# Kernel tuning notes

Measured on AMD Instinct MI355X. Metric: run time of the kernel, lower is better.

The kernel has to match this reference:

```python
import jax, jax.numpy as jnp
import numpy as np
from jax import lax

DT = 0.001            # Euler step_size (forward default)
STEPS_PER_OUT = 5     # t spacing 0.005 / dt 0.001 (t grid aligned with step grid)


def setup_inputs() -> dict:
    key = jax.random.key(0)
    ks = jax.random.split(key, 6)
    B, K, C, F, H = 8192, 2, 2, 64, 64
    D = C * F
    x0 = jax.random.normal(ks[0], (B, K, C, F), dtype=jnp.float32)
    t = jnp.arange(51, dtype=jnp.float32) * 0.005  # 51 output times, aligned to dt grid
    # Kaiming-ish small init so tanh stays in a sane range over 250 Euler steps
    W1 = jax.random.normal(ks[1], (D, H), dtype=jnp.float32) / jnp.sqrt(jnp.float32(D))
    b1 = jax.random.normal(ks[2], (H,), dtype=jnp.float32) * 0.01
    W2 = jax.random.normal(ks[3], (H, D), dtype=jnp.float32) / jnp.sqrt(jnp.float32(H))
    b2 = jax.random.normal(ks[4], (D,), dtype=jnp.float32) * 0.01
    return {"x0": x0, "t": t, "W1": W1, "b1": b1, "W2": W2, "b2": b2}


def reference(x0, t, W1, b1, W2, b2):
    B, K, C, F = x0.shape
    T = t.shape[0]

    def dydt(y):  # tiny 2-layer tanh MLP derivative, y: [B, C*F]
        return jnp.tanh(y @ W1 + b1) @ W2 + b2

    def euler_substep(i, y):
        return y + DT * dydt(y)

    def interval(y, _):
        # STEPS_PER_OUT fixed Euler steps between consecutive output times
        y = lax.fori_loop(0, STEPS_PER_OUT, euler_substep, y)
        return y, y

    y0 = x0.reshape(B, K, C * F)[:, 0]            # flatten(start_dim=-2) then [:, 0]
    _, ys = lax.scan(interval, y0, None, length=T - 1)  # [T-1, B, D]
    out = jnp.concatenate([y0[None], ys], axis=0)       # [T, B, D]
    out = jnp.transpose(out, (1, 0, 2))                 # permute(1,0,2) -> [B, T, D]
    return out.reshape(B, T, C, F)                      # unflatten -> [B, T, C, F]
```

## Files before the change

### kernel.cpp

```cpp
#include <hip/hip_runtime.h>
#include <hip/hip_bf16.h>


typedef __attribute__((ext_vector_type(8))) short bf16x8;
typedef __attribute__((ext_vector_type(4))) float floatx4;

static __device__ __forceinline__ short f2bf(float f) {
    return __builtin_bit_cast(short, (__bf16)f);
}

static __device__ __forceinline__ unsigned pack2(float a, float b) {
    unsigned short lo = __builtin_bit_cast(unsigned short, (__bf16)a);
    unsigned short hi = __builtin_bit_cast(unsigned short, (__bf16)b);
    return (unsigned)lo | ((unsigned)hi << 16);
}

static __device__ __forceinline__ float tanh_fast(float x) {
    float e = __expf(2.0f * x);
    return 1.0f - 2.0f * __builtin_amdgcn_rcpf(1.0f + e);
}

#define YP 136
#define HP 72

__global__ __launch_bounds__(256, 1) void node_kernel(
    const float* __restrict__ x0, const float* __restrict__ W1,
    const float* __restrict__ b1, const float* __restrict__ W2,
    const float* __restrict__ b2, float* __restrict__ out)
{
    __shared__ __align__(16) unsigned short Yld[16 * YP];
    __shared__ __align__(16) unsigned short Hld[16 * HP];

    const int tid  = threadIdx.x;
    const int w    = tid >> 6;
    const int lane = tid & 63;
    const int n    = lane & 15;
    const int q    = lane >> 4;
    const int row  = (blockIdx.x << 4) + n;

    bf16x8 w1f[4];
    #pragma unroll
    for (int kt = 0; kt < 4; ++kt) {
        const int m  = w * 16 + n;
        const int k0 = kt * 32 + q * 8;
        bf16x8 v;
        #pragma unroll
        for (int j = 0; j < 8; ++j) v[j] = f2bf(W1[(k0 + j) * 64 + m]);
        w1f[kt] = v;
    }
    bf16x8 w2f[2][2];
    #pragma unroll
    for (int i = 0; i < 2; ++i) {
        #pragma unroll
        for (int kt = 0; kt < 2; ++kt) {
            const int m  = w * 32 + i * 16 + n;
            const int k0 = kt * 32 + q * 8;
            bf16x8 v;
            #pragma unroll
            for (int j = 0; j < 8; ++j) v[j] = f2bf(W2[(k0 + j) * 128 + m]);
            w2f[i][kt] = v;
        }
    }

    floatx4 b1f, b2f[2];
    #pragma unroll
    for (int r = 0; r < 4; ++r) b1f[r] = b1[w * 16 + q * 4 + r];
    #pragma unroll
    for (int i = 0; i < 2; ++i)
        #pragma unroll
        for (int r = 0; r < 4; ++r) b2f[i][r] = b2[w * 32 + i * 16 + q * 4 + r];

    floatx4 y[2];
    #pragma unroll
    for (int i = 0; i < 2; ++i)
        #pragma unroll
        for (int r = 0; r < 4; ++r)
            y[i][r] = x0[row * 256 + w * 32 + i * 16 + q * 4 + r];

    #pragma unroll
    for (int i = 0; i < 2; ++i) {
        uint2 p;
        p.x = pack2(y[i][0], y[i][1]);
        p.y = pack2(y[i][2], y[i][3]);
        *reinterpret_cast<uint2*>(&Yld[n * YP + w * 32 + i * 16 + q * 4]) = p;
        *reinterpret_cast<floatx4*>(out + row * 51 * 128 + w * 32 + i * 16 + q * 4) = y[i];
    }
    __syncthreads();

    for (int ti = 1; ti <= 50; ++ti) {
        #pragma unroll
        for (int ss = 0; ss < 5; ++ss) {
            bf16x8 yb[4];
            #pragma unroll
            for (int kt = 0; kt < 4; ++kt)
                yb[kt] = __builtin_bit_cast(bf16x8,
                    *reinterpret_cast<const uint4*>(&Yld[n * YP + kt * 32 + q * 8]));
            floatx4 accA = b1f;
            floatx4 accB = {0.0f, 0.0f, 0.0f, 0.0f};
            accA = __builtin_amdgcn_mfma_f32_16x16x32_bf16(w1f[0], yb[0], accA, 0, 0, 0);
            accB = __builtin_amdgcn_mfma_f32_16x16x32_bf16(w1f[1], yb[1], accB, 0, 0, 0);
            accA = __builtin_amdgcn_mfma_f32_16x16x32_bf16(w1f[2], yb[2], accA, 0, 0, 0);
            accB = __builtin_amdgcn_mfma_f32_16x16x32_bf16(w1f[3], yb[3], accB, 0, 0, 0);

            {
                float t0 = tanh_fast(accA[0] + accB[0]);
                float t1 = tanh_fast(accA[1] + accB[1]);
                float t2 = tanh_fast(accA[2] + accB[2]);
                float t3 = tanh_fast(accA[3] + accB[3]);
                uint2 p;
                p.x = pack2(t0, t1);
                p.y = pack2(t2, t3);
                *reinterpret_cast<uint2*>(&Hld[n * HP + w * 16 + q * 4]) = p;
            }
            __syncthreads();

            bf16x8 hb[2];
            #pragma unroll
            for (int kt = 0; kt < 2; ++kt)
                hb[kt] = __builtin_bit_cast(bf16x8,
                    *reinterpret_cast<const uint4*>(&Hld[n * HP + kt * 32 + q * 8]));
            floatx4 acc2[2] = { b2f[0], b2f[1] };
            #pragma unroll
            for (int kt = 0; kt < 2; ++kt)
                #pragma unroll
                for (int i = 0; i < 2; ++i)
                    acc2[i] = __builtin_amdgcn_mfma_f32_16x16x32_bf16(
                        w2f[i][kt], hb[kt], acc2[i], 0, 0, 0);

            #pragma unroll
            for (int i = 0; i < 2; ++i) {
                #pragma unroll
                for (int r = 0; r < 4; ++r)
                    y[i][r] = fmaf(0.001f, acc2[i][r], y[i][r]);
                uint2 p;
                p.x = pack2(y[i][0], y[i][1]);
                p.y = pack2(y[i][2], y[i][3]);
                *reinterpret_cast<uint2*>(&Yld[n * YP + w * 32 + i * 16 + q * 4]) = p;
            }
            __syncthreads();
        }
        #pragma unroll
        for (int i = 0; i < 2; ++i)
            *reinterpret_cast<floatx4*>(
                out + row * 51 * 128 + ti * 128 + w * 32 + i * 16 + q * 4) = y[i];
    }
}

extern "C" void kernel_launch(void* const* d_in, const int* in_sizes, int n_in,
                              void* d_out, int out_size, void* d_ws, size_t ws_size,
                              hipStream_t stream) {
    const float* x0 = (const float*)d_in[0];
    const float* W1 = (const float*)d_in[2];
    const float* b1 = (const float*)d_in[3];
    const float* W2 = (const float*)d_in[4];
    const float* b2 = (const float*)d_in[5];
    float* out = (float*)d_out;

    node_kernel<<<dim3(512), dim3(256), 0, stream>>>(x0, W1, b1, W2, b2, out);
}
```

Baseline: 307.5 us.

## Integrate Euler recurrence in hidden space using precomputed W2·W1 product

Rewrites the Euler update in the 64-wide pre-activation space: z_{k+1} = z_k + dt*(tanh(z_k)·W2W1 + b2W1), using a product matrix computed by a new small precompute kernel. The full 128-wide output y is reconstructed only once per output interval from the summed tanh activations, which halves the inner-step MFMA count and drops the per-step Y write. It also adds XOR-swizzled LDS layouts and double-buffered activation storage, which removes one barrier per substep. The trade-offs are an extra kernel launch and different rounding, since the product is rounded to bf16 and the summed activations are stored in bf16.

```diff
diff --git a/kernel.cpp b/kernel.cpp
--- a/kernel.cpp
+++ b/kernel.cpp
@@ -4,6 +4,8 @@
 
 typedef __attribute__((ext_vector_type(8))) short bf16x8;
 typedef __attribute__((ext_vector_type(4))) float floatx4;
+
+__device__ float g_w21[64 * 64 + 64];
 
 static __device__ __forceinline__ short f2bf(float f) {
     return __builtin_bit_cast(short, (__bf16)f);
@@ -20,16 +22,42 @@
     return 1.0f - 2.0f * __builtin_amdgcn_rcpf(1.0f + e);
 }
 
-#define YP 136
-#define HP 72
+__global__ __launch_bounds__(64) void precompute_kernel(
+    const float* __restrict__ W1, const float* __restrict__ W2,
+    const float* __restrict__ b2)
+{
+    const int hout = threadIdx.x;
+    const int hin  = blockIdx.x;
+    float a0 = 0.f, a1 = 0.f, a2 = 0.f, a3 = 0.f;
+    if (hin < 64) {
+        #pragma unroll 4
+        for (int d = 0; d < 128; d += 4) {
+            a0 = fmaf(W2[hin * 128 + d + 0], W1[(d + 0) * 64 + hout], a0);
+            a1 = fmaf(W2[hin * 128 + d + 1], W1[(d + 1) * 64 + hout], a1);
+            a2 = fmaf(W2[hin * 128 + d + 2], W1[(d + 2) * 64 + hout], a2);
+            a3 = fmaf(W2[hin * 128 + d + 3], W1[(d + 3) * 64 + hout], a3);
+        }
+        g_w21[hin * 64 + hout] = (a0 + a1) + (a2 + a3);
+    } else {
+        #pragma unroll 4
+        for (int d = 0; d < 128; d += 4) {
+            a0 = fmaf(b2[d + 0], W1[(d + 0) * 64 + hout], a0);
+            a1 = fmaf(b2[d + 1], W1[(d + 1) * 64 + hout], a1);
+            a2 = fmaf(b2[d + 2], W1[(d + 2) * 64 + hout], a2);
+            a3 = fmaf(b2[d + 3], W1[(d + 3) * 64 + hout], a3);
+        }
+        g_w21[4096 + hout] = (a0 + a1) + (a2 + a3);
+    }
+}
 
 __global__ __launch_bounds__(256, 1) void node_kernel(
     const float* __restrict__ x0, const float* __restrict__ W1,
     const float* __restrict__ b1, const float* __restrict__ W2,
     const float* __restrict__ b2, float* __restrict__ out)
 {
-    __shared__ __align__(16) unsigned short Yld[16 * YP];
-    __shared__ __align__(16) unsigned short Hld[16 * HP];
+    __shared__ __align__(16) unsigned short Ald[2][16 * 64];
+    __shared__ __align__(16) unsigned short Sld[16 * 64];
+    __shared__ __align__(16) unsigned short Yld[16 * 128];
 
     const int tid  = threadIdx.x;
     const int w    = tid >> 6;
@@ -37,16 +65,17 @@
     const int n    = lane & 15;
     const int q    = lane >> 4;
     const int row  = (blockIdx.x << 4) + n;
-
-    bf16x8 w1f[4];
-    #pragma unroll
-    for (int kt = 0; kt < 4; ++kt) {
+    const int swz  = n & 7;
+
+    bf16x8 w21f[2];
+    #pragma unroll
+    for (int kt = 0; kt < 2; ++kt) {
         const int m  = w * 16 + n;
         const int k0 = kt * 32 + q * 8;
         bf16x8 v;
         #pragma unroll
-        for (int j = 0; j < 8; ++j) v[j] = f2bf(W1[(k0 + j) * 64 + m]);
-        w1f[kt] = v;
+        for (int j = 0; j < 8; ++j) v[j] = f2bf(g_w21[(k0 + j) * 64 + m]);
+        w21f[kt] = v;
     }
     bf16x8 w2f[2][2];
     #pragma unroll
@@ -62,13 +91,17 @@
         }
     }
 
-    floatx4 b1f, b2f[2];
-    #pragma unroll
-    for (int r = 0; r < 4; ++r) b1f[r] = b1[w * 16 + q * 4 + r];
+    floatx4 cf, b1f, b2f5[2];
+    #pragma unroll
+    for (int r = 0; r < 4; ++r) {
+        cf[r]  = g_w21[4096 + w * 16 + q * 4 + r];
+        b1f[r] = b1[w * 16 + q * 4 + r];
+    }
     #pragma unroll
     for (int i = 0; i < 2; ++i)
         #pragma unroll
-        for (int r = 0; r < 4; ++r) b2f[i][r] = b2[w * 32 + i * 16 + q * 4 + r];
+        for (int r = 0; r < 4; ++r)
+            b2f5[i][r] = 5.0f * b2[w * 32 + i * 16 + q * 4 + r];
 
     floatx4 y[2];
     #pragma unroll
@@ -79,70 +112,90 @@
 
     #pragma unroll
     for (int i = 0; i < 2; ++i) {
+        const int j0 = 4 * w + 2 * i + (q >> 1);
         uint2 p;
         p.x = pack2(y[i][0], y[i][1]);
         p.y = pack2(y[i][2], y[i][3]);
-        *reinterpret_cast<uint2*>(&Yld[n * YP + w * 32 + i * 16 + q * 4]) = p;
+        *reinterpret_cast<uint2*>(&Yld[n * 128 + (j0 ^ swz) * 8 + (q & 1) * 4]) = p;
         *reinterpret_cast<floatx4*>(out + row * 51 * 128 + w * 32 + i * 16 + q * 4) = y[i];
     }
     __syncthreads();
 
+    floatx4 z = b1f;
+    #pragma unroll
+    for (int kt = 0; kt < 4; ++kt) {
+        bf16x8 yb = __builtin_bit_cast(bf16x8, *reinterpret_cast<const uint4*>(
+            &Yld[n * 128 + ((kt * 4 + q) ^ swz) * 8]));
+        const int m  = w * 16 + n;
+        const int k0 = kt * 32 + q * 8;
+        bf16x8 w1t;
+        #pragma unroll
+        for (int j = 0; j < 8; ++j) w1t[j] = f2bf(W1[(k0 + j) * 64 + m]);
+        z = __builtin_amdgcn_mfma_f32_16x16x32_bf16(w1t, yb, z, 0, 0, 0);
+    }
+
+    floatx4 S = {0.0f, 0.0f, 0.0f, 0.0f};
+
+    const int awr  = n * 64 + (((2 * w + (q >> 1)) ^ swz) * 8) + (q & 1) * 4;
+    const int ard0 = n * 64 + ((q ^ swz) * 8);
+    const int ard1 = n * 64 + (((4 + q) ^ swz) * 8);
+
     for (int ti = 1; ti <= 50; ++ti) {
         #pragma unroll
         for (int ss = 0; ss < 5; ++ss) {
-            bf16x8 yb[4];
-            #pragma unroll
-            for (int kt = 0; kt < 4; ++kt)
-                yb[kt] = __builtin_bit_cast(bf16x8,
-                    *reinterpret_cast<const uint4*>(&Yld[n * YP + kt * 32 + q * 8]));
-            floatx4 accA = b1f;
-            floatx4 accB = {0.0f, 0.0f, 0.0f, 0.0f};
-            accA = __builtin_amdgcn_mfma_f32_16x16x32_bf16(w1f[0], yb[0], accA, 0, 0, 0);
-            accB = __builtin_amdgcn_mfma_f32_16x16x32_bf16(w1f[1], yb[1], accB, 0, 0, 0);
-            accA = __builtin_amdgcn_mfma_f32_16x16x32_bf16(w1f[2], yb[2], accA, 0, 0, 0);
-            accB = __builtin_amdgcn_mfma_f32_16x16x32_bf16(w1f[3], yb[3], accB, 0, 0, 0);
-
-            {
-                float t0 = tanh_fast(accA[0] + accB[0]);
-                float t1 = tanh_fast(accA[1] + accB[1]);
-                float t2 = tanh_fast(accA[2] + accB[2]);
-                float t3 = tanh_fast(accA[3] + accB[3]);
-                uint2 p;
-                p.x = pack2(t0, t1);
-                p.y = pack2(t2, t3);
-                *reinterpret_cast<uint2*>(&Hld[n * HP + w * 16 + q * 4]) = p;
+            const int p = ss & 1;
+            float a0 = tanh_fast(z[0]);
+            float a1 = tanh_fast(z[1]);
+            float a2 = tanh_fast(z[2]);
+            float a3 = tanh_fast(z[3]);
+            S[0] += a0; S[1] += a1; S[2] += a2; S[3] += a3;
+            uint2 pa;
+            pa.x = pack2(a0, a1);
+            pa.y = pack2(a2, a3);
+            *reinterpret_cast<uint2*>(&Ald[p][awr]) = pa;
+            if (ss == 4) {
+                uint2 ps;
+                ps.x = pack2(S[0], S[1]);
+                ps.y = pack2(S[2], S[3]);
+                *reinterpret_cast<uint2*>(&Sld[awr]) = ps;
             }
             __syncthreads();
 
-            bf16x8 hb[2];
+            bf16x8 ab0 = __builtin_bit_cast(bf16x8,
+                *reinterpret_cast<const uint4*>(&Ald[p][ard0]));
+            bf16x8 ab1 = __builtin_bit_cast(bf16x8,
+                *reinterpret_cast<const uint4*>(&Ald[p][ard1]));
+            floatx4 acc = cf;
+            acc = __builtin_amdgcn_mfma_f32_16x16x32_bf16(w21f[0], ab0, acc, 0, 0, 0);
+            acc = __builtin_amdgcn_mfma_f32_16x16x32_bf16(w21f[1], ab1, acc, 0, 0, 0);
             #pragma unroll
-            for (int kt = 0; kt < 2; ++kt)
-                hb[kt] = __builtin_bit_cast(bf16x8,
-                    *reinterpret_cast<const uint4*>(&Hld[n * HP + kt * 32 + q * 8]));
-            floatx4 acc2[2] = { b2f[0], b2f[1] };
-            #pragma unroll
-            for (int kt = 0; kt < 2; ++kt)
+            for (int r = 0; r < 4; ++r) z[r] = fmaf(0.001f, acc[r], z[r]);
+
+            if (ss == 4) {
+                bf16x8 sb0 = __builtin_bit_cast(bf16x8,
+                    *reinterpret_cast<const uint4*>(&Sld[ard0]));
+                bf16x8 sb1 = __builtin_bit_cast(bf16x8,
+                    *reinterpret_cast<const uint4*>(&Sld[ard1]));
+                floatx4 acc2[2] = { b2f5[0], b2f5[1] };
                 #pragma unroll
-                for (int i = 0; i < 2; ++i)
+                for (int i = 0; i < 2; ++i) {
                     acc2[i] = __builtin_amdgcn_mfma_f32_16x16x32_bf16(
-                        w2f[i][kt], hb[kt], acc2[i], 0, 0, 0);
-
-            #pragma unroll
-            for (int i = 0; i < 2; ++i) {
+                        w2f[i][0], sb0, acc2[i], 0, 0, 0);
+                    acc2[i] = __builtin_amdgcn_mfma_f32_16x16x32_bf16(
+                        w2f[i][1], sb1, acc2[i], 0, 0, 0);
+                }
                 #pragma unroll
-                for (int r = 0; r < 4; ++r)
-                    y[i][r] = fmaf(0.001f, acc2[i][r], y[i][r]);
-                uint2 p;
-                p.x = pack2(y[i][0], y[i][1]);
-                p.y = pack2(y[i][2], y[i][3]);
-                *reinterpret_cast<uint2*>(&Yld[n * YP + w * 32 + i * 16 + q * 4]) = p;
+                for (int i = 0; i < 2; ++i) {
+                    #pragma unroll
+                    for (int r = 0; r < 4; ++r)
+                        y[i][r] = fmaf(0.001f, acc2[i][r], y[i][r]);
+                    *reinterpret_cast<floatx4*>(
+                        out + row * 51 * 128 + ti * 128 + w * 32 + i * 16 + q * 4) = y[i];
+                }
+                S = floatx4{0.0f, 0.0f, 0.0f, 0.0f};
+                __syncthreads();
             }
-            __syncthreads();
-        }
-        #pragma unroll
-        for (int i = 0; i < 2; ++i)
-            *reinterpret_cast<floatx4*>(
-                out + row * 51 * 128 + ti * 128 + w * 32 + i * 16 + q * 4) = y[i];
+        }
     }
 }
 
@@ -156,5 +209,6 @@
     const float* b2 = (const float*)d_in[5];
     float* out = (float*)d_out;
 
+    precompute_kernel<<<dim3(65), dim3(64), 0, stream>>>(W1, W2, b2);
     node_kernel<<<dim3(512), dim3(256), 0, stream>>>(x0, W1, b1, W2, b2, out);
 }
```

Result: faster. 262.3 us (-14.7%).
